# Performance work log

Measured on AMD Instinct MI355X. Metric: run time of the kernel, lower is better.

## Reference

```python
import jax, jax.numpy as jnp
import numpy as np

A, B_, C = 270.0, 108.0, 0.154  # f-I transfer params
DT, I_0, TAU, GAMMA = 0.001, 0.334, 0.06, 0.641


def current_to_frequency(I):
    act = A * I - B_
    # freq = act / (1 - exp(-c*act)), with limit 1/c at act == 0
    zero = act == 0
    act_safe = jnp.where(zero, 1.0, act)  # avoid 0/0 in the unselected branch
    denom = 1.0 - jnp.exp(-C * act_safe)
    return jnp.where(zero, 1.0 / C, act_safe / denom)


def setup_inputs() -> dict:
    key = jax.random.key(0)
    k1, k2 = jax.random.split(key)
    Bsz, T = 8192, 2000
    Js, Jt = 0.35, 0.28387
    inp = jax.random.normal(k1, (Bsz, T, 2), dtype=jnp.float32)
    h0 = jax.random.uniform(k2, (1, Bsz, 2), dtype=jnp.float32)
    J = jnp.array([[(Js + Jt) / 2, (Jt - Js) / 2],
                   [(Jt - Js) / 2, (Js + Jt) / 2]], dtype=jnp.float32)
    return {"input": inp, "h0": h0, "J": J, "steps_per_bin": 4}


def reference(input, h0, J, steps_per_bin):
    # input: [B, T, 2], h0: [1, B, 2], J: [2, 2]
    sub_dt = DT / steps_per_bin

    def sub_step(state, _):
        current = state @ J + I_0 + sub_step.inp  # placeholder, replaced below
        return state, None

    def bin_step(state, inp_t):  # inp_t: [B, 2]
        def sub(state, _):
            current = state @ J + I_0 + inp_t
            rate = current_to_frequency(current)
            state = state + sub_dt * (-state / TAU + GAMMA * (1.0 - state) * rate)
            return state, rate
        state, rates = jax.lax.scan(sub, state, None, length=steps_per_bin)
        return state, (state, rates[-1])

    final, (states, rates) = jax.lax.scan(bin_step, h0[0], jnp.swapaxes(input, 0, 1))
    states = jnp.swapaxes(states, 0, 1)  # [B, T, 2]
    rates = jnp.swapaxes(rates, 0, 1)    # [B, T, 2]
    return states, rates, final[None]     # final: [1, B, 2]
```

## Files before the change

### kernel.cpp

```cpp
#include <hip/hip_runtime.h>


#define AF    270.0f
#define BF    108.0f
#define CF    0.154f
#define DTF   0.001f
#define I0F   0.334f
#define TAUF  0.06f
#define GAMF  0.641f
#define LOG2EF 1.44269504088896340736f
#define LN2F   0.69314718055994530942f

#if __has_builtin(__builtin_amdgcn_exp2f)
#define EXP2F(x) __builtin_amdgcn_exp2f(x)
#else
#define EXP2F(x) exp2f(x)
#endif

#if __has_builtin(__builtin_amdgcn_rcpf)
#define RCPF(x) __builtin_amdgcn_rcpf(x)
#else
#define RCPF(x) (1.0f / (x))
#endif

__device__ __forceinline__ float dpp_swap1(float v) {
  return __int_as_float(
      __builtin_amdgcn_mov_dpp(__float_as_int(v), 0xB1, 0xF, 0xF, true));
}

struct Consts {
  float Xs, Xo;
  float P, Q;
  float K1;
  float K2C;
  float INVC;
};

__device__ __forceinline__ void substep(const Consts& c, float xq,
                                        float& s, float& r2) {
  float so = dpp_swap1(s);
  float p  = fmaf(c.Xs, s, xq);
  float x  = fmaf(c.Xo, so, p);
  float e  = EXP2F(x);
  float d  = 1.0f - e;
  float t  = x * RCPF(d);
  r2 = (__builtin_fabsf(x) < 1e-5f) ? -LOG2EF : t;
  float u = fmaf(-s, r2, r2);
  s = fmaf(c.K2C, u, c.K1 * s);
}

template <int SPB>
__device__ __forceinline__ void bin(const Consts& c, int spb, float in,
                                    float& s, float& rt) {
  float xq = fmaf(c.P, in, c.Q);
  float r2 = -LOG2EF;
  if (SPB > 0) {
#pragma unroll
    for (int k = 0; k < SPB; ++k) substep(c, xq, s, r2);
  } else {
    for (int k = 0; k < spb; ++k) substep(c, xq, s, r2);
  }
  rt = c.INVC * r2;
}

template <int SPB>
__device__ __forceinline__ void run_loop(const Consts& c, int spb, int T,
                                         const float* __restrict__ ip,
                                         float* __restrict__ sp,
                                         float* __restrict__ rp, float& s) {
  constexpr int PF = 8;
  const int Tm1 = T - 1;
  float buf[PF];
#pragma unroll
  for (int i = 0; i < PF; ++i) buf[i] = ip[2 * min(i, Tm1)];
  int t0 = 0;
  for (; t0 + PF <= T; t0 += PF) {
#pragma unroll
    for (int j = 0; j < PF; ++j) {
      float nxt = ip[2 * min(t0 + PF + j, Tm1)];
      float rt;
      bin<SPB>(c, spb, buf[j], s, rt);
      const int t = t0 + j;
      sp[2 * t] = s;
      rp[2 * t] = rt;
      buf[j] = nxt;
    }
  }
  for (; t0 < T; ++t0) {
    float rt;
    bin<SPB>(c, spb, ip[2 * t0], s, rt);
    sp[2 * t0] = s;
    rp[2 * t0] = rt;
  }
}

__global__ __launch_bounds__(64, 1)
void murray_kernel(const float* __restrict__ inp, const float* __restrict__ h0,
                   const float* __restrict__ Jm, const int* __restrict__ spb_p,
                   float* __restrict__ out, int B, int T) {
  const int tid = blockIdx.x * 64 + threadIdx.x;
  const int cB = tid >> 1;
  const int u  = tid & 1;
  if (cB >= B) return;
  const int spb = *spb_p;

  const float Jself = u ? Jm[3] : Jm[0];
  const float Joth  = u ? Jm[1] : Jm[2];
  const float sub_dt = DTF / (float)spb;
  const float NC = -CF * LOG2EF;

  Consts c;
  c.Xs = NC * AF * Jself;
  c.Xo = NC * AF * Joth;
  c.P  = NC * AF;
  c.Q  = NC * fmaf(AF, I0F, -BF);
  c.K1 = 1.0f - sub_dt / TAUF;
  c.INVC = -LN2F / CF;
  c.K2C = sub_dt * GAMF * c.INVC;

  float s = h0[2 * cB + u];

  const size_t row = (size_t)(2 * T);
  const float* ip = inp + (size_t)cB * row + u;
  float* sp = out + (size_t)cB * row + u;
  float* rp = out + (size_t)B * row + (size_t)cB * row + u;
  float* fp = out + (size_t)B * row * 2 + (size_t)(2 * cB + u);

  if (spb == 4) {
    run_loop<4>(c, spb, T, ip, sp, rp, s);
  } else {
    run_loop<0>(c, spb, T, ip, sp, rp, s);
  }

  fp[0] = s;
}

extern "C" void kernel_launch(void* const* d_in, const int* in_sizes, int n_in,
                              void* d_out, int out_size, void* d_ws, size_t ws_size,
                              hipStream_t stream) {
  const float* inp = (const float*)d_in[0];
  const float* h0  = (const float*)d_in[1];
  const float* J   = (const float*)d_in[2];
  const int* spb   = (const int*)d_in[3];
  float* out = (float*)d_out;

  const int B = in_sizes[1] / 2;
  const int T = in_sizes[0] / (2 * B);
  const int threads = 2 * B;
  const int blocks = (threads + 63) / 64;

  murray_kernel<<<blocks, 64, 0, stream>>>(inp, h0, J, spb, out, B, T);
}
```

Before: 659.8 us.

## Interleave multiple independent batch rows per thread to hide recurrence latency

Each lane now advances NB (usually 4) independent batch rows, interleaving their substeps so the serial exp/rcp/dpp dependency chains of different rows can overlap. The launch uses a quarter as many threads (B=8192 gives 4096 threads, 64 single-wave blocks). The deep 8-entry input prefetch is replaced by a 2-ahead rolling prefetch. The trade-off is fewer waves on the device, so latency hiding moves from wave-level to instruction-level parallelism. It also uses more registers and issues scattered loads and stores across four rows per lane.

```diff
diff --git a/kernel.cpp b/kernel.cpp
--- a/kernel.cpp
+++ b/kernel.cpp
@@ -49,59 +49,16 @@
   s = fmaf(c.K2C, u, c.K1 * s);
 }
 
-template <int SPB>
-__device__ __forceinline__ void bin(const Consts& c, int spb, float in,
-                                    float& s, float& rt) {
-  float xq = fmaf(c.P, in, c.Q);
-  float r2 = -LOG2EF;
-  if (SPB > 0) {
-#pragma unroll
-    for (int k = 0; k < SPB; ++k) substep(c, xq, s, r2);
-  } else {
-    for (int k = 0; k < spb; ++k) substep(c, xq, s, r2);
-  }
-  rt = c.INVC * r2;
-}
-
-template <int SPB>
-__device__ __forceinline__ void run_loop(const Consts& c, int spb, int T,
-                                         const float* __restrict__ ip,
-                                         float* __restrict__ sp,
-                                         float* __restrict__ rp, float& s) {
-  constexpr int PF = 8;
-  const int Tm1 = T - 1;
-  float buf[PF];
-#pragma unroll
-  for (int i = 0; i < PF; ++i) buf[i] = ip[2 * min(i, Tm1)];
-  int t0 = 0;
-  for (; t0 + PF <= T; t0 += PF) {
-#pragma unroll
-    for (int j = 0; j < PF; ++j) {
-      float nxt = ip[2 * min(t0 + PF + j, Tm1)];
-      float rt;
-      bin<SPB>(c, spb, buf[j], s, rt);
-      const int t = t0 + j;
-      sp[2 * t] = s;
-      rp[2 * t] = rt;
-      buf[j] = nxt;
-    }
-  }
-  for (; t0 < T; ++t0) {
-    float rt;
-    bin<SPB>(c, spb, ip[2 * t0], s, rt);
-    sp[2 * t0] = s;
-    rp[2 * t0] = rt;
-  }
-}
-
+template <int NB>
 __global__ __launch_bounds__(64, 1)
 void murray_kernel(const float* __restrict__ inp, const float* __restrict__ h0,
                    const float* __restrict__ Jm, const int* __restrict__ spb_p,
                    float* __restrict__ out, int B, int T) {
-  const int tid = blockIdx.x * 64 + threadIdx.x;
-  const int cB = tid >> 1;
-  const int u  = tid & 1;
-  if (cB >= B) return;
+  const int glane = blockIdx.x * 64 + threadIdx.x;
+  const int i = glane >> 1;
+  const int u = glane & 1;
+  const int Bp = B / NB;
+  if (i >= Bp) return;
   const int spb = *spb_p;
 
   const float Jself = u ? Jm[3] : Jm[0];
@@ -118,21 +75,63 @@
   c.INVC = -LN2F / CF;
   c.K2C = sub_dt * GAMF * c.INVC;
 
-  float s = h0[2 * cB + u];
-
   const size_t row = (size_t)(2 * T);
-  const float* ip = inp + (size_t)cB * row + u;
-  float* sp = out + (size_t)cB * row + u;
-  float* rp = out + (size_t)B * row + (size_t)cB * row + u;
-  float* fp = out + (size_t)B * row * 2 + (size_t)(2 * cB + u);
-
-  if (spb == 4) {
-    run_loop<4>(c, spb, T, ip, sp, rp, s);
-  } else {
-    run_loop<0>(c, spb, T, ip, sp, rp, s);
+  const size_t rateOfs = (size_t)B * row;
+  size_t base[NB];
+  float s[NB];
+#pragma unroll
+  for (int n = 0; n < NB; ++n) {
+    const int cB = n * Bp + i;
+    base[n] = (size_t)cB * row + (size_t)u;
+    s[n] = h0[2 * cB + u];
   }
 
-  fp[0] = s;
+  const int Tm1 = T - 1;
+  float b0[NB], b1[NB];
+#pragma unroll
+  for (int n = 0; n < NB; ++n) {
+    b0[n] = inp[base[n]];
+    b1[n] = inp[base[n] + (size_t)(2 * (Tm1 > 0 ? 1 : 0))];
+  }
+
+  for (int t = 0; t < T; ++t) {
+    const int tn = (t + 2 < Tm1 ? t + 2 : Tm1);
+    float nxt[NB];
+#pragma unroll
+    for (int n = 0; n < NB; ++n) nxt[n] = inp[base[n] + (size_t)(2 * tn)];
+
+    float xq[NB], r2[NB];
+#pragma unroll
+    for (int n = 0; n < NB; ++n) {
+      xq[n] = fmaf(c.P, b0[n], c.Q);
+      r2[n] = -LOG2EF;
+    }
+    if (spb == 4) {
+#pragma unroll
+      for (int k = 0; k < 4; ++k)
+#pragma unroll
+        for (int n = 0; n < NB; ++n) substep(c, xq[n], s[n], r2[n]);
+    } else {
+      for (int k = 0; k < spb; ++k)
+#pragma unroll
+        for (int n = 0; n < NB; ++n) substep(c, xq[n], s[n], r2[n]);
+    }
+
+    const size_t to = (size_t)(2 * t);
+#pragma unroll
+    for (int n = 0; n < NB; ++n) {
+      out[base[n] + to] = s[n];
+      out[rateOfs + base[n] + to] = c.INVC * r2[n];
+      b0[n] = b1[n];
+      b1[n] = nxt[n];
+    }
+  }
+
+#pragma unroll
+  for (int n = 0; n < NB; ++n) {
+    const int cB = n * Bp + i;
+    out[rateOfs * 2 + (size_t)(2 * cB + u)] = s[n];
+  }
 }
 
 extern "C" void kernel_launch(void* const* d_in, const int* in_sizes, int n_in,
@@ -146,8 +145,16 @@
 
   const int B = in_sizes[1] / 2;
   const int T = in_sizes[0] / (2 * B);
-  const int threads = 2 * B;
+
+  const int NB = (B % 4 == 0) ? 4 : ((B % 2 == 0) ? 2 : 1);
+  const int threads = 2 * (B / NB);
   const int blocks = (threads + 63) / 64;
 
-  murray_kernel<<<blocks, 64, 0, stream>>>(inp, h0, J, spb, out, B, T);
+  if (NB == 4) {
+    murray_kernel<4><<<blocks, 64, 0, stream>>>(inp, h0, J, spb, out, B, T);
+  } else if (NB == 2) {
+    murray_kernel<2><<<blocks, 64, 0, stream>>>(inp, h0, J, spb, out, B, T);
+  } else {
+    murray_kernel<1><<<blocks, 64, 0, stream>>>(inp, h0, J, spb, out, B, T);
+  }
 }
```

Measured after the change: 1.812 ms. 175% more time.

## Carry exponent argument incrementally to shorten recurrence critical path

Applied to the files above, without the earlier changes.

Reformulates the recurrence so the exp2 argument x is carried across substeps and updated linearly from u (and its lane-swapped partner) rather than recomputed from s after the state update. This takes the K1*s multiply and part of the dot product off the serial dependency chain between consecutive exp/rcp evaluations. At each bin boundary x is adjusted by P times the change in input. The cost is extra FMAs and some floating-point drift, since x is now accumulated incrementally instead of recomputed from s each substep.

```diff
diff --git a/kernel.cpp b/kernel.cpp
--- a/kernel.cpp
+++ b/kernel.cpp
@@ -30,35 +30,41 @@
 
 struct Consts {
   float Xs, Xo;
+  float SXU, SXO;
   float P, Q;
-  float K1;
+  float K1, R1T;
   float K2C;
   float INVC;
 };
 
-__device__ __forceinline__ void substep(const Consts& c, float xq,
-                                        float& s, float& r2) {
-  float so = dpp_swap1(s);
-  float p  = fmaf(c.Xs, s, xq);
-  float x  = fmaf(c.Xo, so, p);
+__device__ __forceinline__ void substep(const Consts& c, float xq1,
+                                        float& s, float& x, float& r2) {
   float e  = EXP2F(x);
   float d  = 1.0f - e;
   float t  = x * RCPF(d);
   r2 = (__builtin_fabsf(x) < 1e-5f) ? -LOG2EF : t;
-  float u = fmaf(-s, r2, r2);
-  s = fmaf(c.K2C, u, c.K1 * s);
+  float k1s = c.K1 * s;
+  float inner = fmaf(c.K1, x, xq1);
+  float u  = fmaf(-s, r2, r2);
+  s = fmaf(c.K2C, u, k1s);
+  float du = dpp_swap1(u);
+  float m1 = fmaf(c.SXU, u, inner);
+  x = fmaf(c.SXO, du, m1);
 }
 
 template <int SPB>
 __device__ __forceinline__ void bin(const Consts& c, int spb, float in,
-                                    float& s, float& rt) {
-  float xq = fmaf(c.P, in, c.Q);
+                                    float& s, float& x, float& inprev,
+                                    float& rt) {
+  x = fmaf(c.P, in - inprev, x);
+  inprev = in;
+  float xq1 = c.R1T * fmaf(c.P, in, c.Q);
   float r2 = -LOG2EF;
   if (SPB > 0) {
 #pragma unroll
-    for (int k = 0; k < SPB; ++k) substep(c, xq, s, r2);
+    for (int k = 0; k < SPB; ++k) substep(c, xq1, s, x, r2);
   } else {
-    for (int k = 0; k < spb; ++k) substep(c, xq, s, r2);
+    for (int k = 0; k < spb; ++k) substep(c, xq1, s, x, r2);
   }
   rt = c.INVC * r2;
 }
@@ -67,19 +73,21 @@
 __device__ __forceinline__ void run_loop(const Consts& c, int spb, int T,
                                          const float* __restrict__ ip,
                                          float* __restrict__ sp,
-                                         float* __restrict__ rp, float& s) {
+                                         float* __restrict__ rp,
+                                         float& s, float& x, float& inprev) {
   constexpr int PF = 8;
   const int Tm1 = T - 1;
   float buf[PF];
 #pragma unroll
-  for (int i = 0; i < PF; ++i) buf[i] = ip[2 * min(i, Tm1)];
+  for (int i = 0; i < PF; ++i) buf[i] = ip[2 * (i < Tm1 ? i : Tm1)];
   int t0 = 0;
   for (; t0 + PF <= T; t0 += PF) {
 #pragma unroll
     for (int j = 0; j < PF; ++j) {
-      float nxt = ip[2 * min(t0 + PF + j, Tm1)];
+      const int tn = (t0 + PF + j < Tm1 ? t0 + PF + j : Tm1);
+      float nxt = ip[2 * tn];
       float rt;
-      bin<SPB>(c, spb, buf[j], s, rt);
+      bin<SPB>(c, spb, buf[j], s, x, inprev, rt);
       const int t = t0 + j;
       sp[2 * t] = s;
       rp[2 * t] = rt;
@@ -88,7 +96,7 @@
   }
   for (; t0 < T; ++t0) {
     float rt;
-    bin<SPB>(c, spb, ip[2 * t0], s, rt);
+    bin<SPB>(c, spb, ip[2 * t0], s, x, inprev, rt);
     sp[2 * t0] = s;
     rp[2 * t0] = rt;
   }
@@ -110,15 +118,21 @@
   const float NC = -CF * LOG2EF;
 
   Consts c;
-  c.Xs = NC * AF * Jself;
-  c.Xo = NC * AF * Joth;
-  c.P  = NC * AF;
-  c.Q  = NC * fmaf(AF, I0F, -BF);
-  c.K1 = 1.0f - sub_dt / TAUF;
+  c.Xs  = NC * AF * Jself;
+  c.Xo  = NC * AF * Joth;
+  c.P   = NC * AF;
+  c.Q   = NC * fmaf(AF, I0F, -BF);
+  c.R1T = sub_dt / TAUF;
+  c.K1  = 1.0f - c.R1T;
   c.INVC = -LN2F / CF;
   c.K2C = sub_dt * GAMF * c.INVC;
+  c.SXU = c.Xs * c.K2C;
+  c.SXO = c.Xo * c.K2C;
 
   float s = h0[2 * cB + u];
+  float so = dpp_swap1(s);
+  float x  = fmaf(c.Xs, s, fmaf(c.Xo, so, c.Q));
+  float inprev = 0.0f;
 
   const size_t row = (size_t)(2 * T);
   const float* ip = inp + (size_t)cB * row + u;
@@ -127,9 +141,9 @@
   float* fp = out + (size_t)B * row * 2 + (size_t)(2 * cB + u);
 
   if (spb == 4) {
-    run_loop<4>(c, spb, T, ip, sp, rp, s);
+    run_loop<4>(c, spb, T, ip, sp, rp, s, x, inprev);
   } else {
-    run_loop<0>(c, spb, T, ip, sp, rp, s);
+    run_loop<0>(c, spb, T, ip, sp, rp, s, x, inprev);
   }
 
   fp[0] = s;
```

Result: no change. 659.9 us (+0.0%).
